# Kernel optimization log

Hardware: AMD Instinct MI355X
Metric: run time of the kernel (lower is better)

The kernel has to match this reference:

```python
import jax, jax.numpy as jnp
import numpy as np

N_NODES = 50000
N_EDGES = 800000
D = 128          # node_state_dim
H = 256          # edge hidden / message dim (= 2*D)
NH = 256         # node MLP hidden


def setup_inputs() -> dict:
    key = jax.random.key(0)
    ks = jax.random.split(key, 20)
    s = 0.05
    inp = {
        "node_states": jax.random.normal(ks[0], (N_NODES, D), jnp.float32),
        "edge_features": jax.random.normal(ks[1], (N_EDGES, 1), jnp.float32),
        "from_idx": jax.random.randint(ks[2], (N_EDGES,), 0, N_NODES, jnp.int32),
        "to_idx": jax.random.randint(ks[3], (N_EDGES,), 0, N_NODES, jnp.int32),
        # forward-direction message net: Linear(2D+1 -> H), ReLU, Linear(H -> H)
        "W1": jax.random.normal(ks[4], (2 * D + 1, H), jnp.float32) * s,
        "b1": jnp.zeros((H,), jnp.float32),
        "W2": jax.random.normal(ks[5], (H, H), jnp.float32) * s,
        "b2": jnp.zeros((H,), jnp.float32),
        # reverse-direction message net (separate params)
        "RW1": jax.random.normal(ks[6], (2 * D + 1, H), jnp.float32) * s,
        "Rb1": jnp.zeros((H,), jnp.float32),
        "RW2": jax.random.normal(ks[7], (H, H), jnp.float32) * s,
        "Rb2": jnp.zeros((H,), jnp.float32),
        # node update MLP: Linear(3D -> NH), ReLU, Linear(NH -> D)
        "Wn1": jax.random.normal(ks[8], (3 * D, NH), jnp.float32) * s,
        "bn1": jnp.zeros((NH,), jnp.float32),
        "Wn2": jax.random.normal(ks[9], (NH, D), jnp.float32) * s,
        "bn2": jnp.zeros((D,), jnp.float32),
    }
    return inp


def _mlp2(x, W1, b1, W2, b2):
    return jax.nn.relu(x @ W1 + b1) @ W2 + b2


def reference(node_states, edge_features, from_idx, to_idx,
              W1, b1, W2, b2, RW1, Rb1, RW2, Rb2, Wn1, bn1, Wn2, bn2):
    n_nodes = node_states.shape[0]
    from_states = node_states[from_idx]            # [E, D]
    to_states = node_states[to_idx]                # [E, D]

    # forward direction: messages go to to_idx
    edge_in = jnp.concatenate([from_states, to_states, edge_features], axis=-1)  # [E, 2D+1]
    msgs = _mlp2(edge_in, W1, b1, W2, b2)                                        # [E, H]
    agg = jax.ops.segment_sum(msgs, to_idx, num_segments=n_nodes)                # [N, H]

    # reverse direction: swap roles, aggregate onto from_idx
    redge_in = jnp.concatenate([to_states, from_states, edge_features], axis=-1)
    rmsgs = _mlp2(redge_in, RW1, Rb1, RW2, Rb2)
    agg = agg + jax.ops.segment_sum(rmsgs, from_idx, num_segments=n_nodes)

    # residual node update: MLP on [agg, node_states] -> [N, D]
    upd_in = jnp.concatenate([agg, node_states], axis=-1)                        # [N, 3D]
    return node_states + _mlp2(upd_in, Wn1, bn1, Wn2, bn2)
```

## Files before the change

kernel.cpp:

```cpp
#include <hip/hip_runtime.h>
#include <hip/hip_bf16.h>


typedef __bf16 bf16;
typedef __attribute__((ext_vector_type(8))) __bf16 bf16x8;
typedef __attribute__((ext_vector_type(4))) __bf16 bf16x4v;
typedef __attribute__((ext_vector_type(4))) float floatx4;
typedef __attribute__((ext_vector_type(2))) float floatx2;

#define DD 128
#define HH 256
#define CAPB 1408
#define MAXBINS 1600

__device__ __forceinline__ bf16x8 ns8(const float* __restrict__ NS, int row, int col, int N) {
    bf16x8 v;
    if (row < N) {
        float4 f0 = *(const float4*)&NS[(size_t)row * DD + col];
        float4 f1 = *(const float4*)&NS[(size_t)row * DD + col + 4];
        v[0] = (bf16)f0.x; v[1] = (bf16)f0.y; v[2] = (bf16)f0.z; v[3] = (bf16)f0.w;
        v[4] = (bf16)f1.x; v[5] = (bf16)f1.y; v[6] = (bf16)f1.z; v[7] = (bf16)f1.w;
    } else {
        v = (bf16x8)(bf16)0.0f;
    }
    return v;
}

__global__ void k_prep_wt1(const float* __restrict__ W1, const float* __restrict__ RW1,
                           bf16* __restrict__ Wt1) {
    int idx = blockIdx.x * 256 + threadIdx.x;
    int n = idx >> 7, k = idx & 127;
    float v;
    if (n < 256)      v = W1[k * 256 + n];
    else if (n < 512) v = W1[(128 + k) * 256 + (n - 256)];
    else if (n < 768) v = RW1[k * 256 + (n - 512)];
    else              v = RW1[(128 + k) * 256 + (n - 768)];
    Wt1[idx] = (bf16)v;
}

__global__ void k_prep_wth(const float* __restrict__ W2, const float* __restrict__ RW2,
                           const float* __restrict__ Wn1, bf16* __restrict__ Wth) {
    int k = blockIdx.x, m = threadIdx.x;
    float v;
    if (k < 512) {
        const float* Wsrc = (k < 256) ? W2 : RW2;
        int i = k & 255;
        float acc = 0.f;
        for (int j = 0; j < 256; ++j) acc += Wsrc[i * 256 + j] * Wn1[j * 256 + m];
        v = acc;
    } else {
        v = Wn1[(256 + k - 512) * 256 + m];
    }
    Wth[m * 640 + k] = (bf16)v;
}

__global__ void k_prep_uru(const float* __restrict__ b2, const float* __restrict__ Rb2,
                           const float* __restrict__ Wn1, float* __restrict__ u,
                           float* __restrict__ ru) {
    int m = threadIdx.x;
    float a = 0.f, b = 0.f;
    for (int j = 0; j < 256; ++j) {
        float w = Wn1[j * 256 + m];
        a += b2[j] * w;
        b += Rb2[j] * w;
    }
    u[m] = a;
    ru[m] = b;
}

__global__ void k_prep_wt2(const float* __restrict__ Wn2, bf16* __restrict__ Wt2) {
    int idx = blockIdx.x * 256 + threadIdx.x;
    int n = idx >> 8, k = idx & 255;
    Wt2[idx] = (bf16)Wn2[k * 128 + n];
}

__global__ __launch_bounds__(256) void k_bins(
    const int* __restrict__ from_idx, const int* __restrict__ to_idx,
    const float* __restrict__ ef, int* __restrict__ gcur,
    int2* __restrict__ binbuf, int E, int NP, int NBINS) {
    __shared__ int hist[MAXBINS];
    __shared__ int base[MAXBINS];
    const int t = threadIdx.x;
    const int NBF = NP >> 6;
    for (int i = t; i < NBINS; i += 256) hist[i] = 0;
    __syncthreads();
    const int e0 = blockIdx.x * 2048;
    int f[8], tt[8]; float w[8]; bool valid[8];
#pragma unroll
    for (int q = 0; q < 8; ++q) {
        int e = e0 + q * 256 + t;
        valid[q] = e < E;
        int ec = valid[q] ? e : 0;
        f[q] = from_idx[ec]; tt[q] = to_idx[ec]; w[q] = ef[ec];
    }
#pragma unroll
    for (int q = 0; q < 8; ++q) {
        if (valid[q]) {
            atomicAdd(&hist[tt[q] >> 6], 1);
            atomicAdd(&hist[NBF + (f[q] >> 6)], 1);
        }
    }
    __syncthreads();
    for (int i = t; i < NBINS; i += 256) {
        int h = hist[i];
        base[i] = h ? atomicAdd(&gcur[i], h) : 0;
        hist[i] = 0;
    }
    __syncthreads();
#pragma unroll
    for (int q = 0; q < 8; ++q) {
        if (valid[q]) {
            int wb = __float_as_int(w[q]);
            int b1 = tt[q] >> 6;
            int r1 = base[b1] + atomicAdd(&hist[b1], 1);
            if (r1 < CAPB)
                binbuf[(size_t)b1 * CAPB + r1] = make_int2(((tt[q] & 63) << 17) | f[q], wb);
            int b2 = NBF + (f[q] >> 6);
            int r2 = base[b2] + atomicAdd(&hist[b2], 1);
            if (r2 < CAPB)
                binbuf[(size_t)b2 * CAPB + r2] = make_int2(((f[q] & 63) << 17) | tt[q], wb);
        }
    }
}

__global__ __launch_bounds__(256) void k_proj(const float* __restrict__ NS,
                                              const bf16* __restrict__ Wt,
                                              unsigned char* __restrict__ Pn,
                                              bf16* __restrict__ Pf, int N) {
    __shared__ __align__(16) bf16 As[2][64][40];
    __shared__ __align__(16) bf16 Bs[2][64][40];
    const int tid = threadIdx.x;
    const int wv = tid >> 6, lane = tid & 63;
    const int l15 = lane & 15, quad = lane >> 4;
    const int row0 = blockIdx.y * 64, col0 = blockIdx.x * 64;
    const int srow = tid >> 2, kc = (tid & 3) * 8;
    floatx4 acc[4] = {};
    for (int k0 = 0; k0 < DD; k0 += 64) {
        bf16x8 av0 = ns8(NS, row0 + srow, k0 + kc, N);
        bf16x8 av1 = ns8(NS, row0 + srow, k0 + 32 + kc, N);
        bf16x8 bv0 = *(const bf16x8*)&Wt[(size_t)(col0 + srow) * DD + k0 + kc];
        bf16x8 bv1 = *(const bf16x8*)&Wt[(size_t)(col0 + srow) * DD + k0 + 32 + kc];
        __syncthreads();
        *(bf16x8*)&As[0][srow][kc] = av0;
        *(bf16x8*)&As[1][srow][kc] = av1;
        *(bf16x8*)&Bs[0][srow][kc] = bv0;
        *(bf16x8*)&Bs[1][srow][kc] = bv1;
        __syncthreads();
#pragma unroll
        for (int h = 0; h < 2; ++h) {
            bf16x8 bfr = *(const bf16x8*)&Bs[h][wv * 16 + l15][quad * 8];
#pragma unroll
            for (int r = 0; r < 4; ++r) {
                bf16x8 afr = *(const bf16x8*)&As[h][r * 16 + l15][quad * 8];
                acc[r] = __builtin_amdgcn_mfma_f32_16x16x32_bf16(afr, bfr, acc[r], 0, 0, 0);
            }
        }
    }
    const int ocol = col0 + wv * 16 + l15;
    const int ch = ocol & 255;
    const int half = (ocol >> 9) & 1;
    const bool isNbr = ((ocol >> 8) & 1) == 0;
#pragma unroll
    for (int r = 0; r < 4; ++r)
#pragma unroll
        for (int i = 0; i < 4; ++i) {
            int orow = row0 + r * 16 + quad * 4 + i;
            float v = acc[r][i];
            if (isNbr) {
                int pk = __builtin_amdgcn_cvt_pk_fp8_f32(v, v, 0, false);
                Pn[(size_t)orow * 512 + half * 256 + ch] = (unsigned char)(pk & 0xFF);
            } else {
                Pf[(size_t)orow * 512 + half * 256 + ch] = (bf16)v;
            }
        }
}

__global__ __launch_bounds__(256) void k_aggf(
    const unsigned char* __restrict__ Pn, const bf16* __restrict__ Pf,
    const int2* __restrict__ binbuf, const int* __restrict__ gcnt,
    const float* __restrict__ W1, const float* __restrict__ b1,
    const float* __restrict__ RW1, const float* __restrict__ Rb1,
    bf16* __restrict__ S_to, bf16* __restrict__ S_fr,
    int* __restrict__ deg, int NP) {
    __shared__ int hist[64], kstart[64], cur[64], scanbuf[64];
    __shared__ int2 srec[CAPB];
    const int b = blockIdx.x, t = threadIdx.x;
    const int NBF = NP >> 6;
    const bool rev = b >= NBF;
    const int node0 = (rev ? b - NBF : b) << 6;
    int cnt = gcnt[b]; if (cnt > CAPB) cnt = CAPB;
    const int2* bin = binbuf + (size_t)b * CAPB;
    if (t < 64) hist[t] = 0;
    __syncthreads();
    for (int i = t; i < cnt; i += 256)
        atomicAdd(&hist[((unsigned)bin[i].x) >> 17], 1);
    __syncthreads();
    if (t < 64) scanbuf[t] = hist[t];
    __syncthreads();
    for (int d = 1; d < 64; d <<= 1) {
        int v = (t < 64 && t >= d) ? scanbuf[t - d] : 0;
        __syncthreads();
        if (t < 64) scanbuf[t] += v;
        __syncthreads();
    }
    if (t < 64) { kstart[t] = scanbuf[t] - hist[t]; cur[t] = scanbuf[t] - hist[t]; }
    __syncthreads();
    for (int i = t; i < cnt; i += 256) {
        int2 r = bin[i];
        int rk = atomicAdd(&cur[((unsigned)r.x) >> 17], 1);
        srec[rk] = r;
    }
    __syncthreads();
    const int wv = t >> 6, lane = t & 63, c = lane * 4;
    const int fixoff = rev ? 256 : 0;
    const int nbroff = rev ? 256 : 0;
    const float* bb = rev ? Rb1 : b1;
    const float* wl = (rev ? RW1 : W1) + 65536;
    float4 bv = *(const float4*)&bb[c];
    float4 wv4 = *(const float4*)&wl[c];
    bf16* Sarr = rev ? S_fr : S_to;
    for (int key = wv; key < 64; key += 4) {
        int node = node0 + key;
        bf16x4v pf = *(const bf16x4v*)&Pf[(size_t)node * 512 + fixoff + c];
        float fx0 = (float)pf[0] + bv.x;
        float fx1 = (float)pf[1] + bv.y;
        float fx2 = (float)pf[2] + bv.z;
        float fx3 = (float)pf[3] + bv.w;
        int beg = kstart[key], kc2 = hist[key], end = beg + kc2;
        float a0 = 0.f, a1 = 0.f, a2 = 0.f, a3 = 0.f;
        int j = beg;
        for (; j + 4 <= end; j += 4) {
            int2 r0 = srec[j], r1 = srec[j + 1], r2 = srec[j + 2], r3 = srec[j + 3];
            int q0 = *(const int*)&Pn[(size_t)(r0.x & 0x1FFFF) * 512 + nbroff + c];
            int q1 = *(const int*)&Pn[(size_t)(r1.x & 0x1FFFF) * 512 + nbroff + c];
            int q2 = *(const int*)&Pn[(size_t)(r2.x & 0x1FFFF) * 512 + nbroff + c];
            int q3 = *(const int*)&Pn[(size_t)(r3.x & 0x1FFFF) * 512 + nbroff + c];
#pragma unroll
            for (int z = 0; z < 4; ++z) {
                int qq = z == 0 ? q0 : z == 1 ? q1 : z == 2 ? q2 : q3;
                float w = __int_as_float(z == 0 ? r0.y : z == 1 ? r1.y : z == 2 ? r2.y : r3.y);
                floatx2 lo = __builtin_amdgcn_cvt_pk_f32_fp8(qq, false);
                floatx2 hi = __builtin_amdgcn_cvt_pk_f32_fp8(qq, true);
                a0 += fmaxf(fx0 + lo.x + w * wv4.x, 0.f);
                a1 += fmaxf(fx1 + lo.y + w * wv4.y, 0.f);
                a2 += fmaxf(fx2 + hi.x + w * wv4.z, 0.f);
                a3 += fmaxf(fx3 + hi.y + w * wv4.w, 0.f);
            }
        }
        for (; j < end; ++j) {
            int2 r = srec[j];
            int qq = *(const int*)&Pn[(size_t)(r.x & 0x1FFFF) * 512 + nbroff + c];
            float w = __int_as_float(r.y);
            floatx2 lo = __builtin_amdgcn_cvt_pk_f32_fp8(qq, false);
            floatx2 hi = __builtin_amdgcn_cvt_pk_f32_fp8(qq, true);
            a0 += fmaxf(fx0 + lo.x + w * wv4.x, 0.f);
            a1 += fmaxf(fx1 + lo.y + w * wv4.y, 0.f);
            a2 += fmaxf(fx2 + hi.x + w * wv4.z, 0.f);
            a3 += fmaxf(fx3 + hi.y + w * wv4.w, 0.f);
        }
        bf16x4v o;
        o[0] = (bf16)a0; o[1] = (bf16)a1; o[2] = (bf16)a2; o[3] = (bf16)a3;
        *(bf16x4v*)&Sarr[(size_t)node * 256 + c] = o;
        if (lane == 0) deg[(rev ? NP : 0) + node] = kc2;
    }
}

__global__ __launch_bounds__(256) void k_hid(
    const bf16* __restrict__ S_to, const bf16* __restrict__ S_fr,
    const float* __restrict__ NS, const bf16* __restrict__ Wth,
    const float* __restrict__ u, const float* __restrict__ ru,
    const float* __restrict__ bn1, const int* __restrict__ deg,
    bf16* __restrict__ Hid, int NP, int N) {
    __shared__ __align__(16) bf16 As[2][64][40];
    __shared__ __align__(16) bf16 Bs[2][64][40];
    const int tid = threadIdx.x;
    const int wv = tid >> 6, lane = tid & 63;
    const int l15 = lane & 15, quad = lane >> 4;
    const int row0 = blockIdx.y * 64, col0 = blockIdx.x * 64;
    const int srow = tid >> 2, kc = (tid & 3) * 8;
    floatx4 acc[4] = {};
    const int arow = row0 + srow;
    for (int k0 = 0; k0 < 640; k0 += 64) {
        bf16x8 av0, av1;
        if (k0 < 512) {
            const bf16* S = (k0 < 256) ? S_to : S_fr;
            int cb = (k0 & 255) + kc;
            av0 = *(const bf16x8*)&S[(size_t)arow * 256 + cb];
            av1 = *(const bf16x8*)&S[(size_t)arow * 256 + cb + 32];
        } else {
            int cb = (k0 - 512) + kc;
            av0 = ns8(NS, arow, cb, N);
            av1 = ns8(NS, arow, cb + 32, N);
        }
        bf16x8 bv0 = *(const bf16x8*)&Wth[(size_t)(col0 + srow) * 640 + k0 + kc];
        bf16x8 bv1 = *(const bf16x8*)&Wth[(size_t)(col0 + srow) * 640 + k0 + 32 + kc];
        __syncthreads();
        *(bf16x8*)&As[0][srow][kc] = av0;
        *(bf16x8*)&As[1][srow][kc] = av1;
        *(bf16x8*)&Bs[0][srow][kc] = bv0;
        *(bf16x8*)&Bs[1][srow][kc] = bv1;
        __syncthreads();
#pragma unroll
        for (int h = 0; h < 2; ++h) {
            bf16x8 bfr = *(const bf16x8*)&Bs[h][wv * 16 + l15][quad * 8];
#pragma unroll
            for (int r = 0; r < 4; ++r) {
                bf16x8 afr = *(const bf16x8*)&As[h][r * 16 + l15][quad * 8];
                acc[r] = __builtin_amdgcn_mfma_f32_16x16x32_bf16(afr, bfr, acc[r], 0, 0, 0);
            }
        }
    }
    const int ocol = col0 + wv * 16 + l15;
    float uc = u[ocol], rc = ru[ocol], bc = bn1[ocol];
#pragma unroll
    for (int r = 0; r < 4; ++r)
#pragma unroll
        for (int i = 0; i < 4; ++i) {
            int orow = row0 + r * 16 + quad * 4 + i;
            int din = deg[orow];
            int dout = deg[NP + orow];
            float v = acc[r][i] + (float)din * uc + (float)dout * rc + bc;
            Hid[(size_t)orow * 256 + ocol] = (bf16)fmaxf(v, 0.f);
        }
}

__global__ __launch_bounds__(256) void k_out(
    const bf16* __restrict__ Hid, const bf16* __restrict__ Wt2,
    const float* __restrict__ NS, const float* __restrict__ bn2,
    float* __restrict__ out, int N) {
    __shared__ __align__(16) bf16 As[2][64][40];
    __shared__ __align__(16) bf16 Bs[2][64][40];
    const int tid = threadIdx.x;
    const int wv = tid >> 6, lane = tid & 63;
    const int l15 = lane & 15, quad = lane >> 4;
    const int row0 = blockIdx.y * 64, col0 = blockIdx.x * 64;
    const int srow = tid >> 2, kc = (tid & 3) * 8;
    floatx4 acc[4] = {};
    for (int k0 = 0; k0 < HH; k0 += 64) {
        bf16x8 av0 = *(const bf16x8*)&Hid[(size_t)(row0 + srow) * HH + k0 + kc];
        bf16x8 av1 = *(const bf16x8*)&Hid[(size_t)(row0 + srow) * HH + k0 + 32 + kc];
        bf16x8 bv0 = *(const bf16x8*)&Wt2[(size_t)(col0 + srow) * HH + k0 + kc];
        bf16x8 bv1 = *(const bf16x8*)&Wt2[(size_t)(col0 + srow) * HH + k0 + 32 + kc];
        __syncthreads();
        *(bf16x8*)&As[0][srow][kc] = av0;
        *(bf16x8*)&As[1][srow][kc] = av1;
        *(bf16x8*)&Bs[0][srow][kc] = bv0;
        *(bf16x8*)&Bs[1][srow][kc] = bv1;
        __syncthreads();
#pragma unroll
        for (int h = 0; h < 2; ++h) {
            bf16x8 bfr = *(const bf16x8*)&Bs[h][wv * 16 + l15][quad * 8];
#pragma unroll
            for (int r = 0; r < 4; ++r) {
                bf16x8 afr = *(const bf16x8*)&As[h][r * 16 + l15][quad * 8];
                acc[r] = __builtin_amdgcn_mfma_f32_16x16x32_bf16(afr, bfr, acc[r], 0, 0, 0);
            }
        }
    }
    const int ocol = col0 + wv * 16 + l15;
    float bb = bn2[ocol];
#pragma unroll
    for (int r = 0; r < 4; ++r)
#pragma unroll
        for (int i = 0; i < 4; ++i) {
            int orow = row0 + r * 16 + quad * 4 + i;
            if (orow < N)
                out[(size_t)orow * DD + ocol] = acc[r][i] + bb + NS[(size_t)orow * DD + ocol];
        }
}

extern "C" void kernel_launch(void* const* d_in, const int* in_sizes, int n_in,
                              void* d_out, int out_size, void* d_ws, size_t ws_size,
                              hipStream_t stream) {
    const float* NS   = (const float*)d_in[0];
    const float* ef   = (const float*)d_in[1];
    const int* from_idx = (const int*)d_in[2];
    const int* to_idx   = (const int*)d_in[3];
    const float* W1  = (const float*)d_in[4];
    const float* b1  = (const float*)d_in[5];
    const float* W2  = (const float*)d_in[6];
    const float* b2  = (const float*)d_in[7];
    const float* RW1 = (const float*)d_in[8];
    const float* Rb1 = (const float*)d_in[9];
    const float* RW2 = (const float*)d_in[10];
    const float* Rb2 = (const float*)d_in[11];
    const float* Wn1 = (const float*)d_in[12];
    const float* bn1 = (const float*)d_in[13];
    const float* Wn2 = (const float*)d_in[14];
    const float* bn2 = (const float*)d_in[15];

    const int N  = in_sizes[0] / DD;
    const int E  = in_sizes[2];
    const int NP = ((N + 63) / 64) * 64;
    const int MB = NP / 64;
    const int NBF = NP / 64;
    const int NBINS = 2 * NBF;

    char* base = (char*)d_ws;
    size_t off_b = 0;
    auto alloc = [&](size_t b) { size_t o = off_b; off_b += (b + 255) & ~(size_t)255; return o; };
    unsigned char* Pn = (unsigned char*)(base + alloc((size_t)NP * 512));
    bf16* Hid  = (bf16*)Pn;
    bf16* Pf   = (bf16*)(base + alloc((size_t)NP * 512 * 2));
    bf16* S_to = (bf16*)(base + alloc((size_t)NP * 256 * 2));
    bf16* S_fr = (bf16*)(base + alloc((size_t)NP * 256 * 2));
    int* deg   = (int*)(base + alloc((size_t)2 * NP * 4));
    int* gcur  = (int*)(base + alloc((size_t)NBINS * 4));
    int2* binbuf = (int2*)(base + alloc((size_t)NBINS * CAPB * 8));
    bf16* Wt1 = (bf16*)(base + alloc(1024 * 128 * 2));
    bf16* Wth = (bf16*)(base + alloc(256 * 640 * 2));
    bf16* Wt2 = (bf16*)(base + alloc(128 * 256 * 2));
    float* u  = (float*)(base + alloc(256 * 4));
    float* ru = (float*)(base + alloc(256 * 4));

    hipMemsetAsync(gcur, 0, (size_t)NBINS * 4, stream);

    k_prep_wt1<<<512, 256, 0, stream>>>(W1, RW1, Wt1);
    k_prep_wth<<<640, 256, 0, stream>>>(W2, RW2, Wn1, Wth);
    k_prep_uru<<<1, 256, 0, stream>>>(b2, Rb2, Wn1, u, ru);
    k_prep_wt2<<<128, 256, 0, stream>>>(Wn2, Wt2);

    k_bins<<<(E + 2047) / 2048, 256, 0, stream>>>(from_idx, to_idx, ef, gcur,
                                                  binbuf, E, NP, NBINS);

    k_proj<<<dim3(16, MB), 256, 0, stream>>>(NS, Wt1, Pn, Pf, N);
    k_aggf<<<NBINS, 256, 0, stream>>>(Pn, Pf, binbuf, gcur, W1, b1, RW1, Rb1,
                                      S_to, S_fr, deg, NP);
    k_hid<<<dim3(4, MB), 256, 0, stream>>>(S_to, S_fr, NS, Wth, u, ru, bn1, deg,
                                           Hid, NP, N);
    k_out<<<dim3(2, MB), 256, 0, stream>>>(Hid, Wt2, NS, bn2, (float*)d_out, N);
}
```

Before: 361.3 us.

## Fuse node MLP layers into one kernel and merge weight-prep kernels

Merges the two node-update GEMM kernels into one k_node kernel. Each block computes a 64-row tile of the full 256-wide hidden layer, keeps it in shared memory as bf16, then runs the second GEMM against Wt2 read directly from global memory. This removes the Hid round trip through global memory and one launch. The four weight-prep kernels are also folded into a single launch. In exchange the grid is 4x smaller with more accumulators per thread (64 floats for the first GEMM), which may lower occupancy. The K step is also halved, so there are more sync iterations.

```diff
diff --git a/kernel.cpp b/kernel.cpp
--- a/kernel.cpp
+++ b/kernel.cpp
@@ -26,52 +26,51 @@
     return v;
 }
 
-__global__ void k_prep_wt1(const float* __restrict__ W1, const float* __restrict__ RW1,
-                           bf16* __restrict__ Wt1) {
-    int idx = blockIdx.x * 256 + threadIdx.x;
-    int n = idx >> 7, k = idx & 127;
-    float v;
-    if (n < 256)      v = W1[k * 256 + n];
-    else if (n < 512) v = W1[(128 + k) * 256 + (n - 256)];
-    else if (n < 768) v = RW1[k * 256 + (n - 512)];
-    else              v = RW1[(128 + k) * 256 + (n - 768)];
-    Wt1[idx] = (bf16)v;
-}
-
-__global__ void k_prep_wth(const float* __restrict__ W2, const float* __restrict__ RW2,
-                           const float* __restrict__ Wn1, bf16* __restrict__ Wth) {
-    int k = blockIdx.x, m = threadIdx.x;
-    float v;
-    if (k < 512) {
-        const float* Wsrc = (k < 256) ? W2 : RW2;
-        int i = k & 255;
-        float acc = 0.f;
-        for (int j = 0; j < 256; ++j) acc += Wsrc[i * 256 + j] * Wn1[j * 256 + m];
-        v = acc;
+__global__ void k_prep(const float* __restrict__ W1, const float* __restrict__ RW1,
+                       const float* __restrict__ W2, const float* __restrict__ RW2,
+                       const float* __restrict__ Wn1, const float* __restrict__ Wn2,
+                       const float* __restrict__ b2, const float* __restrict__ Rb2,
+                       bf16* __restrict__ Wt1, bf16* __restrict__ Wth,
+                       bf16* __restrict__ Wt2, float* __restrict__ u,
+                       float* __restrict__ ru) {
+    const int b = blockIdx.x, t = threadIdx.x;
+    if (b < 512) {
+        int idx = b * 256 + t;
+        int n = idx >> 7, k = idx & 127;
+        float v;
+        if (n < 256)      v = W1[k * 256 + n];
+        else if (n < 512) v = W1[(128 + k) * 256 + (n - 256)];
+        else if (n < 768) v = RW1[k * 256 + (n - 512)];
+        else              v = RW1[(128 + k) * 256 + (n - 768)];
+        Wt1[idx] = (bf16)v;
+    } else if (b < 1152) {
+        int k = b - 512, m = t;
+        float v;
+        if (k < 512) {
+            const float* Wsrc = (k < 256) ? W2 : RW2;
+            int i = k & 255;
+            float acc = 0.f;
+            for (int j = 0; j < 256; ++j) acc += Wsrc[i * 256 + j] * Wn1[j * 256 + m];
+            v = acc;
+        } else {
+            v = Wn1[(256 + k - 512) * 256 + m];
+        }
+        Wth[m * 640 + k] = (bf16)v;
+    } else if (b < 1280) {
+        int idx = (b - 1152) * 256 + t;
+        int n = idx >> 8, k = idx & 255;
+        Wt2[idx] = (bf16)Wn2[k * 128 + n];
     } else {
-        v = Wn1[(256 + k - 512) * 256 + m];
-    }
-    Wth[m * 640 + k] = (bf16)v;
-}
-
-__global__ void k_prep_uru(const float* __restrict__ b2, const float* __restrict__ Rb2,
-                           const float* __restrict__ Wn1, float* __restrict__ u,
-                           float* __restrict__ ru) {
-    int m = threadIdx.x;
-    float a = 0.f, b = 0.f;
-    for (int j = 0; j < 256; ++j) {
-        float w = Wn1[j * 256 + m];
-        a += b2[j] * w;
-        b += Rb2[j] * w;
-    }
-    u[m] = a;
-    ru[m] = b;
-}
-
-__global__ void k_prep_wt2(const float* __restrict__ Wn2, bf16* __restrict__ Wt2) {
-    int idx = blockIdx.x * 256 + threadIdx.x;
-    int n = idx >> 8, k = idx & 255;
-    Wt2[idx] = (bf16)Wn2[k * 128 + n];
+        int m = t;
+        float a = 0.f, bb = 0.f;
+        for (int j = 0; j < 256; ++j) {
+            float w = Wn1[j * 256 + m];
+            a += b2[j] * w;
+            bb += Rb2[j] * w;
+        }
+        u[m] = a;
+        ru[m] = bb;
+    }
 }
 
 __global__ __launch_bounds__(256) void k_bins(
@@ -265,108 +264,96 @@
     }
 }
 
-__global__ __launch_bounds__(256) void k_hid(
+__global__ __launch_bounds__(256) void k_node(
     const bf16* __restrict__ S_to, const bf16* __restrict__ S_fr,
     const float* __restrict__ NS, const bf16* __restrict__ Wth,
+    const bf16* __restrict__ Wt2,
     const float* __restrict__ u, const float* __restrict__ ru,
-    const float* __restrict__ bn1, const int* __restrict__ deg,
-    bf16* __restrict__ Hid, int NP, int N) {
-    __shared__ __align__(16) bf16 As[2][64][40];
-    __shared__ __align__(16) bf16 Bs[2][64][40];
+    const float* __restrict__ bn1, const float* __restrict__ bn2,
+    const int* __restrict__ deg, float* __restrict__ out, int NP, int N) {
+    __shared__ __align__(16) unsigned char smem[33792];
+    bf16 (*As)[40]  = (bf16(*)[40])smem;
+    bf16 (*Bs)[40]  = (bf16(*)[40])(smem + 5120);
+    bf16 (*Hs)[264] = (bf16(*)[264])smem;
     const int tid = threadIdx.x;
     const int wv = tid >> 6, lane = tid & 63;
     const int l15 = lane & 15, quad = lane >> 4;
-    const int row0 = blockIdx.y * 64, col0 = blockIdx.x * 64;
+    const int row0 = blockIdx.x * 64;
     const int srow = tid >> 2, kc = (tid & 3) * 8;
-    floatx4 acc[4] = {};
+    floatx4 acc[4][4] = {};
     const int arow = row0 + srow;
-    for (int k0 = 0; k0 < 640; k0 += 64) {
-        bf16x8 av0, av1;
+    for (int k0 = 0; k0 < 640; k0 += 32) {
+        bf16x8 av;
         if (k0 < 512) {
             const bf16* S = (k0 < 256) ? S_to : S_fr;
-            int cb = (k0 & 255) + kc;
-            av0 = *(const bf16x8*)&S[(size_t)arow * 256 + cb];
-            av1 = *(const bf16x8*)&S[(size_t)arow * 256 + cb + 32];
+            av = *(const bf16x8*)&S[(size_t)arow * 256 + (k0 & 255) + kc];
         } else {
-            int cb = (k0 - 512) + kc;
-            av0 = ns8(NS, arow, cb, N);
-            av1 = ns8(NS, arow, cb + 32, N);
-        }
-        bf16x8 bv0 = *(const bf16x8*)&Wth[(size_t)(col0 + srow) * 640 + k0 + kc];
-        bf16x8 bv1 = *(const bf16x8*)&Wth[(size_t)(col0 + srow) * 640 + k0 + 32 + kc];
-        __syncthreads();
-        *(bf16x8*)&As[0][srow][kc] = av0;
-        *(bf16x8*)&As[1][srow][kc] = av1;
-        *(bf16x8*)&Bs[0][srow][kc] = bv0;
-        *(bf16x8*)&Bs[1][srow][kc] = bv1;
-        __syncthreads();
-#pragma unroll
-        for (int h = 0; h < 2; ++h) {
-            bf16x8 bfr = *(const bf16x8*)&Bs[h][wv * 16 + l15][quad * 8];
+            av = ns8(NS, arow, (k0 - 512) + kc, N);
+        }
+        bf16x8 bv[4];
+#pragma unroll
+        for (int j = 0; j < 4; ++j)
+            bv[j] = *(const bf16x8*)&Wth[(size_t)(srow + 64 * j) * 640 + k0 + kc];
+        __syncthreads();
+        *(bf16x8*)&As[srow][kc] = av;
+#pragma unroll
+        for (int j = 0; j < 4; ++j)
+            *(bf16x8*)&Bs[srow + 64 * j][kc] = bv[j];
+        __syncthreads();
+#pragma unroll
+        for (int s = 0; s < 4; ++s) {
+            bf16x8 bfr = *(const bf16x8*)&Bs[wv * 64 + s * 16 + l15][quad * 8];
 #pragma unroll
             for (int r = 0; r < 4; ++r) {
-                bf16x8 afr = *(const bf16x8*)&As[h][r * 16 + l15][quad * 8];
-                acc[r] = __builtin_amdgcn_mfma_f32_16x16x32_bf16(afr, bfr, acc[r], 0, 0, 0);
-            }
-        }
-    }
-    const int ocol = col0 + wv * 16 + l15;
-    float uc = u[ocol], rc = ru[ocol], bc = bn1[ocol];
-#pragma unroll
-    for (int r = 0; r < 4; ++r)
-#pragma unroll
-        for (int i = 0; i < 4; ++i) {
-            int orow = row0 + r * 16 + quad * 4 + i;
-            int din = deg[orow];
-            int dout = deg[NP + orow];
-            float v = acc[r][i] + (float)din * uc + (float)dout * rc + bc;
-            Hid[(size_t)orow * 256 + ocol] = (bf16)fmaxf(v, 0.f);
-        }
-}
-
-__global__ __launch_bounds__(256) void k_out(
-    const bf16* __restrict__ Hid, const bf16* __restrict__ Wt2,
-    const float* __restrict__ NS, const float* __restrict__ bn2,
-    float* __restrict__ out, int N) {
-    __shared__ __align__(16) bf16 As[2][64][40];
-    __shared__ __align__(16) bf16 Bs[2][64][40];
-    const int tid = threadIdx.x;
-    const int wv = tid >> 6, lane = tid & 63;
-    const int l15 = lane & 15, quad = lane >> 4;
-    const int row0 = blockIdx.y * 64, col0 = blockIdx.x * 64;
-    const int srow = tid >> 2, kc = (tid & 3) * 8;
-    floatx4 acc[4] = {};
-    for (int k0 = 0; k0 < HH; k0 += 64) {
-        bf16x8 av0 = *(const bf16x8*)&Hid[(size_t)(row0 + srow) * HH + k0 + kc];
-        bf16x8 av1 = *(const bf16x8*)&Hid[(size_t)(row0 + srow) * HH + k0 + 32 + kc];
-        bf16x8 bv0 = *(const bf16x8*)&Wt2[(size_t)(col0 + srow) * HH + k0 + kc];
-        bf16x8 bv1 = *(const bf16x8*)&Wt2[(size_t)(col0 + srow) * HH + k0 + 32 + kc];
-        __syncthreads();
-        *(bf16x8*)&As[0][srow][kc] = av0;
-        *(bf16x8*)&As[1][srow][kc] = av1;
-        *(bf16x8*)&Bs[0][srow][kc] = bv0;
-        *(bf16x8*)&Bs[1][srow][kc] = bv1;
-        __syncthreads();
-#pragma unroll
-        for (int h = 0; h < 2; ++h) {
-            bf16x8 bfr = *(const bf16x8*)&Bs[h][wv * 16 + l15][quad * 8];
-#pragma unroll
-            for (int r = 0; r < 4; ++r) {
-                bf16x8 afr = *(const bf16x8*)&As[h][r * 16 + l15][quad * 8];
-                acc[r] = __builtin_amdgcn_mfma_f32_16x16x32_bf16(afr, bfr, acc[r], 0, 0, 0);
-            }
-        }
-    }
-    const int ocol = col0 + wv * 16 + l15;
-    float bb = bn2[ocol];
-#pragma unroll
-    for (int r = 0; r < 4; ++r)
-#pragma unroll
-        for (int i = 0; i < 4; ++i) {
-            int orow = row0 + r * 16 + quad * 4 + i;
-            if (orow < N)
-                out[(size_t)orow * DD + ocol] = acc[r][i] + bb + NS[(size_t)orow * DD + ocol];
-        }
+                bf16x8 afr = *(const bf16x8*)&As[r * 16 + l15][quad * 8];
+                acc[s][r] = __builtin_amdgcn_mfma_f32_16x16x32_bf16(afr, bfr, acc[s][r], 0, 0, 0);
+            }
+        }
+    }
+    __syncthreads();
+#pragma unroll
+    for (int s = 0; s < 4; ++s) {
+        int col = wv * 64 + s * 16 + l15;
+        float uc = u[col], rc = ru[col], bc = bn1[col];
+#pragma unroll
+        for (int r = 0; r < 4; ++r)
+#pragma unroll
+            for (int i = 0; i < 4; ++i) {
+                int row = r * 16 + quad * 4 + i;
+                float v = acc[s][r][i] + (float)deg[row0 + row] * uc
+                        + (float)deg[NP + row0 + row] * rc + bc;
+                Hs[row][col] = (bf16)fmaxf(v, 0.f);
+            }
+    }
+    __syncthreads();
+    floatx4 acc2[2][4] = {};
+    for (int k0 = 0; k0 < HH; k0 += 32) {
+        bf16x8 afr[4];
+#pragma unroll
+        for (int r = 0; r < 4; ++r)
+            afr[r] = *(const bf16x8*)&Hs[r * 16 + l15][k0 + quad * 8];
+#pragma unroll
+        for (int s = 0; s < 2; ++s) {
+            int col = wv * 32 + s * 16 + l15;
+            bf16x8 bfr = *(const bf16x8*)&Wt2[(size_t)col * HH + k0 + quad * 8];
+#pragma unroll
+            for (int r = 0; r < 4; ++r)
+                acc2[s][r] = __builtin_amdgcn_mfma_f32_16x16x32_bf16(afr[r], bfr, acc2[s][r], 0, 0, 0);
+        }
+    }
+#pragma unroll
+    for (int s = 0; s < 2; ++s) {
+        int ocol = wv * 32 + s * 16 + l15;
+        float bb = bn2[ocol];
+#pragma unroll
+        for (int r = 0; r < 4; ++r)
+#pragma unroll
+            for (int i = 0; i < 4; ++i) {
+                int orow = row0 + r * 16 + quad * 4 + i;
+                if (orow < N)
+                    out[(size_t)orow * DD + ocol] = acc2[s][r][i] + bb + NS[(size_t)orow * DD + ocol];
+            }
+    }
 }
 
 extern "C" void kernel_launch(void* const* d_in, const int* in_sizes, int n_in,
@@ -400,7 +387,6 @@
     size_t off_b = 0;
     auto alloc = [&](size_t b) { size_t o = off_b; off_b += (b + 255) & ~(size_t)255; return o; };
     unsigned char* Pn = (unsigned char*)(base + alloc((size_t)NP * 512));
-    bf16* Hid  = (bf16*)Pn;
     bf16* Pf   = (bf16*)(base + alloc((size_t)NP * 512 * 2));
     bf16* S_to = (bf16*)(base + alloc((size_t)NP * 256 * 2));
     bf16* S_fr = (bf16*)(base + alloc((size_t)NP * 256 * 2));
@@ -415,10 +401,8 @@
 
     hipMemsetAsync(gcur, 0, (size_t)NBINS * 4, stream);
 
-    k_prep_wt1<<<512, 256, 0, stream>>>(W1, RW1, Wt1);
-    k_prep_wth<<<640, 256, 0, stream>>>(W2, RW2, Wn1, Wth);
-    k_prep_uru<<<1, 256, 0, stream>>>(b2, Rb2, Wn1, u, ru);
-    k_prep_wt2<<<128, 256, 0, stream>>>(Wn2, Wt2);
+    k_prep<<<1281, 256, 0, stream>>>(W1, RW1, W2, RW2, Wn1, Wn2, b2, Rb2,
+                                     Wt1, Wth, Wt2, u, ru);
 
     k_bins<<<(E + 2047) / 2048, 256, 0, stream>>>(from_idx, to_idx, ef, gcur,
                                                   binbuf, E, NP, NBINS);
@@ -426,7 +410,6 @@
     k_proj<<<dim3(16, MB), 256, 0, stream>>>(NS, Wt1, Pn, Pf, N);
     k_aggf<<<NBINS, 256, 0, stream>>>(Pn, Pf, binbuf, gcur, W1, b1, RW1, Rb1,
                                       S_to, S_fr, deg, NP);
-    k_hid<<<dim3(4, MB), 256, 0, stream>>>(S_to, S_fr, NS, Wth, u, ru, bn1, deg,
-                                           Hid, NP, N);
-    k_out<<<dim3(2, MB), 256, 0, stream>>>(Hid, Wt2, NS, bn2, (float*)d_out, N);
-}
+    k_node<<<MB, 256, 0, stream>>>(S_to, S_fr, NS, Wth, Wt2, u, ru, bn1, bn2,
+                                   deg, (float*)d_out, NP, N);
+}
```

Result: faster. 343.0 us (-5.1%).
